# Kernel optimization log

Measured on AMD Instinct MI355X. Metric: run time of the kernel, lower is better.

## Reference

```python
import jax, jax.numpy as jnp
import numpy as np

B = 8192
FEAT = 7680
HID = 512
LOC = 4
N_SCENES = 72


def setup_inputs() -> dict:
    key = jax.random.key(0)
    ks = jax.random.split(key, 12)
    s = lambda fan_in: 1.0 / np.sqrt(fan_in)
    inp = {
        "feat": jax.random.normal(ks[0], (B, FEAT), dtype=jnp.float32),
        "scene_idx": jax.random.randint(ks[1], (B,), 0, N_SCENES, dtype=jnp.int64),
        # visual_fc1: Linear(7680 -> 512)  (torch layout: W[out, in])
        "W1": jax.random.uniform(ks[2], (HID, FEAT), jnp.float32, -s(FEAT), s(FEAT)),
        "b1": jax.random.uniform(ks[3], (HID,), jnp.float32, -s(FEAT), s(FEAT)),
        # localization_fc: Linear(512 -> 512), ReLU, Linear(512 -> 4)
        "W2": jax.random.uniform(ks[4], (HID, HID), jnp.float32, -s(HID), s(HID)),
        "b2": jax.random.uniform(ks[5], (HID,), jnp.float32, -s(HID), s(HID)),
        "W3": jax.random.uniform(ks[6], (LOC, HID), jnp.float32, -s(HID), s(HID)),
        "b3": jax.random.uniform(ks[7], (LOC,), jnp.float32, -s(HID), s(HID)),
        # per-scene 2x2 affine (with bias) and 2x2 rotation (no bias)
        "xyW": jax.random.uniform(ks[8], (N_SCENES, 2, 2), jnp.float32, -s(2), s(2)),
        "xyb": jax.random.uniform(ks[9], (N_SCENES, 2), jnp.float32, -s(2), s(2)),
        "tW": jax.random.uniform(ks[10], (N_SCENES, 2, 2), jnp.float32, -s(2), s(2)),
    }
    return inp


def reference(feat, scene_idx, W1, b1, W2, b2, W3, b3, xyW, xyb, tW):
    # visual_fc1: Flatten (already flat) -> Linear -> ReLU
    h = jax.nn.relu(feat @ W1.T + b1)                 # [B, HID]
    # localization_fc: Linear -> ReLU -> Linear
    h = jax.nn.relu(h @ W2.T + b2)                    # [B, HID]
    shared = h @ W3.T + b3                            # [B, 4]
    # per-scene routed 2x2 linears: gather weights per sample, apply, "scatter" is
    # implicit since every row gets exactly one scene's transform.
    sidx = scene_idx.astype(jnp.int32)
    Wxy = xyW[sidx]                                   # [B, 2, 2]
    bxy = xyb[sidx]                                   # [B, 2]
    Wt = tW[sidx]                                     # [B, 2, 2]
    xy = jnp.einsum("boi,bi->bo", Wxy, shared[:, :2]) + bxy
    t = jnp.einsum("boi,bi->bo", Wt, shared[:, 2:])
    return jnp.concatenate([xy, t], axis=1)           # [B, 4]
```

## Files before the change

kernel.cpp:

```cpp
#include <hip/hip_runtime.h>
#include <stdint.h>
#include <stddef.h>

#define BROWS 8192
#define FEATK 7680
#define HIDN  512

typedef __attribute__((ext_vector_type(8))) __bf16 bf16x8;
typedef __attribute__((ext_vector_type(4))) float f32x4;

__device__ __forceinline__ unsigned short f2b(float f) {
  unsigned int u = __float_as_uint(f);
  unsigned int r = (u + 0x7FFFu + ((u >> 16) & 1u)) >> 16;
  return (unsigned short)r;
}

__global__ void cvt_kernel(const float* __restrict__ src, unsigned short* __restrict__ dst, int n4) {
  int i = blockIdx.x * blockDim.x + threadIdx.x;
  int stride = gridDim.x * blockDim.x;
  for (; i < n4; i += stride) {
    float4 v = ((const float4*)src)[i];
    ushort4 o;
    o.x = f2b(v.x); o.y = f2b(v.y); o.z = f2b(v.z); o.w = f2b(v.w);
    ((ushort4*)dst)[i] = o;
  }
}

#define K1_BM 64
#define K1_BK 32

__global__ __launch_bounds__(256, 2) void gemm1_fused_splitk(
    const float* __restrict__ A,
    const unsigned short* __restrict__ Bm,
    float* __restrict__ P,
    int M, int N, int K, int klen) {
  __shared__ unsigned short As[K1_BM * K1_BK];
  __shared__ unsigned short Bs[HIDN * K1_BK];

  const int tid  = threadIdx.x;
  const int lane = tid & 63;
  const int wid  = tid >> 6;
  const int l16  = lane & 15;
  const int quad = lane >> 4;

  const int rowBase = blockIdx.y * K1_BM;
  const int k_begin = blockIdx.x * klen;

  f32x4 acc[4][8] = {};

  for (int k0 = k_begin; k0 < k_begin + klen; k0 += K1_BK) {
#pragma unroll
    for (int it = 0; it < 2; ++it) {
      int c   = it * 256 + tid;
      int row = c >> 3;
      int kq  = c & 7;
      const float4* ga = (const float4*)(A + (size_t)(rowBase + row) * K + k0 + kq * 4);
      float4 v = *ga;
      ushort4 o;
      o.x = f2b(v.x); o.y = f2b(v.y); o.z = f2b(v.z); o.w = f2b(v.w);
      *(ushort4*)(As + row * K1_BK + kq * 4) = o;
    }
#pragma unroll
    for (int it = 0; it < 8; ++it) {
      int cb  = it * 256 + wid * 64;
      int c   = cb + lane;
      int row = c >> 2;
      int kk  = (c & 3) << 3;
      const unsigned short* gb = Bm + (size_t)row * K + (k0 + kk);
      __builtin_amdgcn_global_load_lds(
          (const __attribute__((address_space(1))) void*)gb,
          (__attribute__((address_space(3))) void*)(Bs + (size_t)cb * 8), 16, 0, 0);
    }
    __syncthreads();

    bf16x8 af[4], bfr[8];
#pragma unroll
    for (int mt = 0; mt < 4; ++mt)
      af[mt] = *(const bf16x8*)(As + (mt * 16 + l16) * K1_BK + quad * 8);
#pragma unroll
    for (int nt = 0; nt < 8; ++nt)
      bfr[nt] = *(const bf16x8*)(Bs + (wid * 128 + nt * 16 + l16) * K1_BK + quad * 8);
#pragma unroll
    for (int mt = 0; mt < 4; ++mt)
#pragma unroll
      for (int nt = 0; nt < 8; ++nt)
        acc[mt][nt] = __builtin_amdgcn_mfma_f32_16x16x32_bf16(af[mt], bfr[nt], acc[mt][nt], 0, 0, 0);
    __syncthreads();
  }

  float* outp = P + (size_t)blockIdx.x * M * N;
#pragma unroll
  for (int mt = 0; mt < 4; ++mt) {
#pragma unroll
    for (int r = 0; r < 4; ++r) {
      int row = rowBase + mt * 16 + quad * 4 + r;
      float* cp = outp + (size_t)row * N + wid * 128 + l16;
#pragma unroll
      for (int nt = 0; nt < 8; ++nt) cp[nt * 16] = acc[mt][nt][r];
    }
  }
}

__global__ __launch_bounds__(256) void reduce4_bias_relu(
    const float* __restrict__ P, const float* __restrict__ bias,
    unsigned short* __restrict__ H, int MN4, int N4) {
  int i = blockIdx.x * blockDim.x + threadIdx.x;
  if (i >= MN4) return;
  const float4* p = (const float4*)P;
  float4 a = p[i];
  float4 b = p[i + MN4];
  float4 c = p[i + 2 * MN4];
  float4 d = p[i + 3 * MN4];
  float4 bs = ((const float4*)bias)[i % N4];
  ushort4 o;
  o.x = f2b(fmaxf(a.x + b.x + c.x + d.x + bs.x, 0.0f));
  o.y = f2b(fmaxf(a.y + b.y + c.y + d.y + bs.y, 0.0f));
  o.z = f2b(fmaxf(a.z + b.z + c.z + d.z + bs.z, 0.0f));
  o.w = f2b(fmaxf(a.w + b.w + c.w + d.w + bs.w, 0.0f));
  ((ushort4*)H)[i] = o;
}

#define BM 128
#define BN 128
#define BK 64

__global__ __launch_bounds__(256, 2) void gemm_bt_bias_relu(
    const unsigned short* __restrict__ A,
    const unsigned short* __restrict__ Bm,
    const float* __restrict__ bias,
    unsigned short* __restrict__ C,
    int M, int N, int K) {
  __shared__ unsigned short As[BM * BK];
  __shared__ unsigned short Bs[BN * BK];
  const int tid  = threadIdx.x;
  const int lane = tid & 63;
  const int wid  = tid >> 6;
  const int wm   = wid >> 1;
  const int wn   = wid & 1;
  const int l16  = lane & 15;
  const int quad = lane >> 4;
  const int rowBase = blockIdx.y * BM;
  const int colBase = blockIdx.x * BN;

  f32x4 acc[4][4] = {};

  for (int k0 = 0; k0 < K; k0 += BK) {
#pragma unroll
    for (int it = 0; it < 4; ++it) {
      int cb = it * 256 + wid * 64;
      int c  = cb + lane;
      int row = c >> 3;
      int kk  = (c & 7) << 3;
      const unsigned short* ga = A + (size_t)(rowBase + row) * K + (k0 + kk);
      __builtin_amdgcn_global_load_lds(
          (const __attribute__((address_space(1))) void*)ga,
          (__attribute__((address_space(3))) void*)(As + (size_t)cb * 8), 16, 0, 0);
      const unsigned short* gb = Bm + (size_t)(colBase + row) * K + (k0 + kk);
      __builtin_amdgcn_global_load_lds(
          (const __attribute__((address_space(1))) void*)gb,
          (__attribute__((address_space(3))) void*)(Bs + (size_t)cb * 8), 16, 0, 0);
    }
    __syncthreads();
#pragma unroll
    for (int kk = 0; kk < BK; kk += 32) {
      bf16x8 af[4], bfr[4];
#pragma unroll
      for (int mt = 0; mt < 4; ++mt)
        af[mt] = *(const bf16x8*)(As + (wm * 64 + mt * 16 + l16) * BK + kk + quad * 8);
#pragma unroll
      for (int nt = 0; nt < 4; ++nt)
        bfr[nt] = *(const bf16x8*)(Bs + (wn * 64 + nt * 16 + l16) * BK + kk + quad * 8);
#pragma unroll
      for (int mt = 0; mt < 4; ++mt)
#pragma unroll
        for (int nt = 0; nt < 4; ++nt)
          acc[mt][nt] = __builtin_amdgcn_mfma_f32_16x16x32_bf16(af[mt], bfr[nt], acc[mt][nt], 0, 0, 0);
    }
    __syncthreads();
  }

  float bvals[4];
#pragma unroll
  for (int nt = 0; nt < 4; ++nt) bvals[nt] = bias[colBase + wn * 64 + nt * 16 + l16];
#pragma unroll
  for (int mt = 0; mt < 4; ++mt) {
#pragma unroll
    for (int r = 0; r < 4; ++r) {
      int row = rowBase + wm * 64 + mt * 16 + quad * 4 + r;
      unsigned short* cp = C + (size_t)row * N + colBase + wn * 64 + l16;
#pragma unroll
      for (int nt = 0; nt < 4; ++nt) {
        float v = fmaxf(acc[mt][nt][r] + bvals[nt], 0.0f);
        cp[nt * 16] = f2b(v);
      }
    }
  }
}

__global__ __launch_bounds__(256) void head_kernel(
    const unsigned short* __restrict__ h2,
    const float* __restrict__ W3,
    const float* __restrict__ b3,
    const int* __restrict__ sidx,
    const float* __restrict__ xyW,
    const float* __restrict__ xyb,
    const float* __restrict__ tW,
    float* __restrict__ out) {
  int wave = (blockIdx.x * blockDim.x + threadIdx.x) >> 6;
  int lane = threadIdx.x & 63;
  if (wave >= BROWS) return;

  bf16x8 hv = *(const bf16x8*)(h2 + (size_t)wave * 512 + lane * 8);
  float hf[8];
#pragma unroll
  for (int j = 0; j < 8; ++j) hf[j] = (float)hv[j];

  float s[4];
#pragma unroll
  for (int o = 0; o < 4; ++o) {
    const float* wrow = W3 + o * 512 + lane * 8;
    float4 w0 = ((const float4*)wrow)[0];
    float4 w1 = ((const float4*)wrow)[1];
    float a = hf[0] * w0.x + hf[1] * w0.y + hf[2] * w0.z + hf[3] * w0.w +
              hf[4] * w1.x + hf[5] * w1.y + hf[6] * w1.z + hf[7] * w1.w;
#pragma unroll
    for (int off = 32; off > 0; off >>= 1) a += __shfl_down(a, off, 64);
    s[o] = a;
  }

  if (lane == 0) {
#pragma unroll
    for (int o = 0; o < 4; ++o) s[o] += b3[o];
    int sc = sidx[wave];
    const float* wx = xyW + sc * 4;
    const float* bx = xyb + sc * 2;
    const float* wt = tW + sc * 4;
    float o0 = wx[0] * s[0] + wx[1] * s[1] + bx[0];
    float o1 = wx[2] * s[0] + wx[3] * s[1] + bx[1];
    float o2 = wt[0] * s[2] + wt[1] * s[3];
    float o3 = wt[2] * s[2] + wt[3] * s[3];
    ((float4*)out)[wave] = make_float4(o0, o1, o2, o3);
  }
}

#define WS_W1B   0UL
#define WS_W2B   7864320UL
#define WS_H1    8388608UL
#define WS_H2    16777216UL
#define WS_PART  25165824UL
#define WS_NEED  92274688UL

extern "C" void kernel_launch(void* const* d_in, const int* in_sizes, int n_in,
                              void* d_out, int out_size, void* d_ws, size_t ws_size,
                              hipStream_t stream) {
  const float* feat = (const float*)d_in[0];
  const int*   sidx = (const int*)d_in[1];
  const float* W1   = (const float*)d_in[2];
  const float* b1   = (const float*)d_in[3];
  const float* W2   = (const float*)d_in[4];
  const float* b2   = (const float*)d_in[5];
  const float* W3   = (const float*)d_in[6];
  const float* b3   = (const float*)d_in[7];
  const float* xyW  = (const float*)d_in[8];
  const float* xyb  = (const float*)d_in[9];
  const float* tW   = (const float*)d_in[10];
  float* out = (float*)d_out;

  if (ws_size < WS_NEED) return;

  char* ws = (char*)d_ws;
  unsigned short* W1B  = (unsigned short*)(ws + WS_W1B);
  unsigned short* W2B  = (unsigned short*)(ws + WS_W2B);
  unsigned short* h1   = (unsigned short*)(ws + WS_H1);
  unsigned short* h2   = (unsigned short*)(ws + WS_H2);
  float*          part = (float*)(ws + WS_PART);

  cvt_kernel<<<512, 256, 0, stream>>>(W1, W1B, (HIDN * FEATK) / 4);
  cvt_kernel<<<64, 256, 0, stream>>>(W2, W2B, (HIDN * HIDN) / 4);

  gemm1_fused_splitk<<<dim3(4, BROWS / K1_BM), 256, 0, stream>>>(
      feat, W1B, part, BROWS, HIDN, FEATK, FEATK / 4);
  reduce4_bias_relu<<<(BROWS * HIDN / 4 + 255) / 256, 256, 0, stream>>>(
      part, b1, h1, BROWS * HIDN / 4, HIDN / 4);

  gemm_bt_bias_relu<<<dim3(HIDN / BN, BROWS / BM), 256, 0, stream>>>(
      h1, W2B, b2, h2, BROWS, HIDN, HIDN);

  head_kernel<<<(BROWS * 64) / 256, 256, 0, stream>>>(
      h2, W3, b3, sidx, xyW, xyb, tW, out);
}
```

Baseline: 479.0 us.

## Double-buffer LDS tiles in both GEMM kernels to overlap loads with MFMA

Both GEMM kernels now keep two LDS buffers and issue the global loads for the next K-step before computing on the current one. In the split-K first GEMM, the fp32 activation tile is prefetched into registers and converted to bf16 into the alternate buffer after the MFMAs. The aim is to hide global memory latency behind matrix math and to drop one barrier per step. The cost is doubled LDS use and more live registers, which could reduce occupancy.

```diff
diff --git a/kernel.cpp b/kernel.cpp
--- a/kernel.cpp
+++ b/kernel.cpp
@@ -34,8 +34,8 @@
     const unsigned short* __restrict__ Bm,
     float* __restrict__ P,
     int M, int N, int K, int klen) {
-  __shared__ unsigned short As[K1_BM * K1_BK];
-  __shared__ unsigned short Bs[HIDN * K1_BK];
+  __shared__ unsigned short As[2][K1_BM * K1_BK];
+  __shared__ unsigned short Bs[2][HIDN * K1_BK];
 
   const int tid  = threadIdx.x;
   const int lane = tid & 63;
@@ -45,47 +45,80 @@
 
   const int rowBase = blockIdx.y * K1_BM;
   const int k_begin = blockIdx.x * klen;
+  const int nsteps  = klen / K1_BK;
+
+  const int arow = tid >> 3;
+  const int akq  = tid & 7;
+  const int brow0 = (wid * 64 + lane) >> 2;
+  const int bkk   = (lane & 3) << 3;
 
   f32x4 acc[4][8] = {};
 
-  for (int k0 = k_begin; k0 < k_begin + klen; k0 += K1_BK) {
+  {
+    const int k0 = k_begin;
 #pragma unroll
     for (int it = 0; it < 2; ++it) {
-      int c   = it * 256 + tid;
-      int row = c >> 3;
-      int kq  = c & 7;
-      const float4* ga = (const float4*)(A + (size_t)(rowBase + row) * K + k0 + kq * 4);
-      float4 v = *ga;
+      int row = it * 32 + arow;
+      float4 v = *(const float4*)(A + (size_t)(rowBase + row) * K + k0 + akq * 4);
       ushort4 o;
       o.x = f2b(v.x); o.y = f2b(v.y); o.z = f2b(v.z); o.w = f2b(v.w);
-      *(ushort4*)(As + row * K1_BK + kq * 4) = o;
+      *(ushort4*)(&As[0][row * K1_BK + akq * 4]) = o;
     }
 #pragma unroll
     for (int it = 0; it < 8; ++it) {
       int cb  = it * 256 + wid * 64;
-      int c   = cb + lane;
-      int row = c >> 2;
-      int kk  = (c & 3) << 3;
-      const unsigned short* gb = Bm + (size_t)row * K + (k0 + kk);
+      int row = it * 64 + brow0;
+      const unsigned short* gb = Bm + (size_t)row * K + (k0 + bkk);
       __builtin_amdgcn_global_load_lds(
           (const __attribute__((address_space(1))) void*)gb,
-          (__attribute__((address_space(3))) void*)(Bs + (size_t)cb * 8), 16, 0, 0);
-    }
-    __syncthreads();
+          (__attribute__((address_space(3))) void*)(&Bs[0][cb * 8]), 16, 0, 0);
+    }
+  }
+  __syncthreads();
+
+  int cur = 0;
+  for (int t = 0; t < nsteps; ++t) {
+    const int nxt = cur ^ 1;
+    const bool hasNext = (t + 1 < nsteps);
+    float4 va0, va1;
+
+    if (hasNext) {
+      const int kn = k_begin + (t + 1) * K1_BK;
+      va0 = *(const float4*)(A + (size_t)(rowBase + arow) * K + kn + akq * 4);
+      va1 = *(const float4*)(A + (size_t)(rowBase + 32 + arow) * K + kn + akq * 4);
+#pragma unroll
+      for (int it = 0; it < 8; ++it) {
+        int cb  = it * 256 + wid * 64;
+        int row = it * 64 + brow0;
+        const unsigned short* gb = Bm + (size_t)row * K + (kn + bkk);
+        __builtin_amdgcn_global_load_lds(
+            (const __attribute__((address_space(1))) void*)gb,
+            (__attribute__((address_space(3))) void*)(&Bs[nxt][cb * 8]), 16, 0, 0);
+      }
+    }
 
     bf16x8 af[4], bfr[8];
 #pragma unroll
     for (int mt = 0; mt < 4; ++mt)
-      af[mt] = *(const bf16x8*)(As + (mt * 16 + l16) * K1_BK + quad * 8);
+      af[mt] = *(const bf16x8*)(&As[cur][(mt * 16 + l16) * K1_BK + quad * 8]);
 #pragma unroll
     for (int nt = 0; nt < 8; ++nt)
-      bfr[nt] = *(const bf16x8*)(Bs + (wid * 128 + nt * 16 + l16) * K1_BK + quad * 8);
+      bfr[nt] = *(const bf16x8*)(&Bs[cur][(wid * 128 + nt * 16 + l16) * K1_BK + quad * 8]);
 #pragma unroll
     for (int mt = 0; mt < 4; ++mt)
 #pragma unroll
       for (int nt = 0; nt < 8; ++nt)
         acc[mt][nt] = __builtin_amdgcn_mfma_f32_16x16x32_bf16(af[mt], bfr[nt], acc[mt][nt], 0, 0, 0);
+
+    if (hasNext) {
+      ushort4 o0, o1;
+      o0.x = f2b(va0.x); o0.y = f2b(va0.y); o0.z = f2b(va0.z); o0.w = f2b(va0.w);
+      o1.x = f2b(va1.x); o1.y = f2b(va1.y); o1.z = f2b(va1.z); o1.w = f2b(va1.w);
+      *(ushort4*)(&As[nxt][arow * K1_BK + akq * 4]) = o0;
+      *(ushort4*)(&As[nxt][(32 + arow) * K1_BK + akq * 4]) = o1;
+    }
     __syncthreads();
+    cur = nxt;
   }
 
   float* outp = P + (size_t)blockIdx.x * M * N;
@@ -130,8 +163,8 @@
     const float* __restrict__ bias,
     unsigned short* __restrict__ C,
     int M, int N, int K) {
-  __shared__ unsigned short As[BM * BK];
-  __shared__ unsigned short Bs[BN * BK];
+  __shared__ unsigned short As[2][BM * BK];
+  __shared__ unsigned short Bs[2][BN * BK];
   const int tid  = threadIdx.x;
   const int lane = tid & 63;
   const int wid  = tid >> 6;
@@ -142,34 +175,55 @@
   const int rowBase = blockIdx.y * BM;
   const int colBase = blockIdx.x * BN;
 
+  const int srow = tid >> 3;
+  const int skk  = (tid & 7) << 3;
+
   f32x4 acc[4][4] = {};
-
-  for (int k0 = 0; k0 < K; k0 += BK) {
-#pragma unroll
-    for (int it = 0; it < 4; ++it) {
-      int cb = it * 256 + wid * 64;
-      int c  = cb + lane;
-      int row = c >> 3;
-      int kk  = (c & 7) << 3;
-      const unsigned short* ga = A + (size_t)(rowBase + row) * K + (k0 + kk);
-      __builtin_amdgcn_global_load_lds(
-          (const __attribute__((address_space(1))) void*)ga,
-          (__attribute__((address_space(3))) void*)(As + (size_t)cb * 8), 16, 0, 0);
-      const unsigned short* gb = Bm + (size_t)(colBase + row) * K + (k0 + kk);
-      __builtin_amdgcn_global_load_lds(
-          (const __attribute__((address_space(1))) void*)gb,
-          (__attribute__((address_space(3))) void*)(Bs + (size_t)cb * 8), 16, 0, 0);
-    }
-    __syncthreads();
+  const int nsteps = K / BK;
+
+#pragma unroll
+  for (int it = 0; it < 4; ++it) {
+    int cb  = it * 256 + wid * 64;
+    int row = it * 32 + srow;
+    const unsigned short* ga = A + (size_t)(rowBase + row) * K + skk;
+    __builtin_amdgcn_global_load_lds(
+        (const __attribute__((address_space(1))) void*)ga,
+        (__attribute__((address_space(3))) void*)(&As[0][cb * 8]), 16, 0, 0);
+    const unsigned short* gb = Bm + (size_t)(colBase + row) * K + skk;
+    __builtin_amdgcn_global_load_lds(
+        (const __attribute__((address_space(1))) void*)gb,
+        (__attribute__((address_space(3))) void*)(&Bs[0][cb * 8]), 16, 0, 0);
+  }
+  __syncthreads();
+
+  int cur = 0;
+  for (int t = 0; t < nsteps; ++t) {
+    const int nxt = cur ^ 1;
+    if (t + 1 < nsteps) {
+      const int kn = (t + 1) * BK;
+#pragma unroll
+      for (int it = 0; it < 4; ++it) {
+        int cb  = it * 256 + wid * 64;
+        int row = it * 32 + srow;
+        const unsigned short* ga = A + (size_t)(rowBase + row) * K + kn + skk;
+        __builtin_amdgcn_global_load_lds(
+            (const __attribute__((address_space(1))) void*)ga,
+            (__attribute__((address_space(3))) void*)(&As[nxt][cb * 8]), 16, 0, 0);
+        const unsigned short* gb = Bm + (size_t)(colBase + row) * K + kn + skk;
+        __builtin_amdgcn_global_load_lds(
+            (const __attribute__((address_space(1))) void*)gb,
+            (__attribute__((address_space(3))) void*)(&Bs[nxt][cb * 8]), 16, 0, 0);
+      }
+    }
 #pragma unroll
     for (int kk = 0; kk < BK; kk += 32) {
       bf16x8 af[4], bfr[4];
 #pragma unroll
       for (int mt = 0; mt < 4; ++mt)
-        af[mt] = *(const bf16x8*)(As + (wm * 64 + mt * 16 + l16) * BK + kk + quad * 8);
+        af[mt] = *(const bf16x8*)(&As[cur][(wm * 64 + mt * 16 + l16) * BK + kk + quad * 8]);
 #pragma unroll
       for (int nt = 0; nt < 4; ++nt)
-        bfr[nt] = *(const bf16x8*)(Bs + (wn * 64 + nt * 16 + l16) * BK + kk + quad * 8);
+        bfr[nt] = *(const bf16x8*)(&Bs[cur][(wn * 64 + nt * 16 + l16) * BK + kk + quad * 8]);
 #pragma unroll
       for (int mt = 0; mt < 4; ++mt)
 #pragma unroll
@@ -177,6 +231,7 @@
           acc[mt][nt] = __builtin_amdgcn_mfma_f32_16x16x32_bf16(af[mt], bfr[nt], acc[mt][nt], 0, 0, 0);
     }
     __syncthreads();
+    cur = nxt;
   }
 
   float bvals[4];
```

Measured after the change: 483.7 us. No clear change (+1.0%).
